# Optimization experiments

Measured on AMD Instinct MI355X. Metric: run time of the kernel, lower is better.

The kernel has to match this reference:

```python
import jax, jax.numpy as jnp
import numpy as np

B, C, H, W = 16, 3, 128, 128
PATCH = 8
E = 512          # embedding_dim
NH = 8           # num_heads
P = 64           # proj_dim
HID = 2048       # hidden_dim
L = 6            # num_layers
COND = 3
PH, PW = H // PATCH, W // PATCH
S = PH * PW + 1  # sequence length (patches + cond token)
INV_SQRT_E = 1.0 / np.float32(np.sqrt(E))

_PARAM_SHAPES = {
    'patch_w': (E, C, PATCH, PATCH), 'patch_b': (E,),
    'cond_w1': (COND, E), 'cond_b1': (E,), 'cond_w2': (E, E), 'cond_b2': (E,),
    'pos_embed': (1, S, E),
    'enc_vp': (L, NH, E, P), 'enc_kp': (L, NH, E, P), 'enc_qh': (L, NH, S, S), 'enc_lift': (L, 1, NH * P, E),
    'enc_ln1g': (L, E), 'enc_ln1b': (L, E),
    'enc_w1': (L, E, HID), 'enc_b1': (L, HID), 'enc_w2': (L, HID, E), 'enc_b2': (L, E),
    'enc_ln2g': (L, E), 'enc_ln2b': (L, E),
    'dec_vp': (L, NH, E, P), 'dec_kp': (L, NH, E, P), 'dec_qh': (L, NH, S, S), 'dec_lift': (L, 1, NH * P, E),
    'dec_ln2g': (L, E), 'dec_ln2b': (L, E),
    'dec_w1': (L, E, HID), 'dec_b1': (L, HID), 'dec_w2': (L, HID, E), 'dec_b2': (L, E),
    'dec_ln3g': (L, E), 'dec_ln3b': (L, E),
    'final_g': (E,), 'final_b': (E,),
    'deconv_w': (E, C, PATCH, PATCH), 'deconv_b': (C,),
}


def setup_inputs() -> dict:
    key = jax.random.key(0)
    inp = {
        'x': jax.random.normal(jax.random.fold_in(key, 1000), (B, C, H, W), jnp.float32),
        'y': jax.random.normal(jax.random.fold_in(key, 1001), (B, COND), jnp.float32),
    }
    for i, (name, shp) in enumerate(_PARAM_SHAPES.items()):
        w = 0.02 * jax.random.normal(jax.random.fold_in(key, i), shp, jnp.float32)
        if name.endswith('g'):  # layernorm gains near 1
            w = w + 1.0
        inp[name] = w
    return inp


def _ln(x, g, b, eps=1e-5):
    m = x.mean(-1, keepdims=True)
    v = ((x - m) ** 2).mean(-1, keepdims=True)
    return (x - m) * jax.lax.rsqrt(v + eps) * g + b


def _mhsa(x, vp, kp, qh, lift):
    # x: (B,S,E); vp/kp: (NH,E,P); qh: (NH,S,S); lift: (1, NH*P, E)
    k = jnp.einsum('bse,hep->bhsp', x, kp)
    v = jnp.einsum('bse,hep->bhsp', x, vp)
    qv = jnp.einsum('hst,bhtp->bhsp', qh, v)
    # a_ts = (qh@V) @ K^T, then transpose(-2,-1): a[t,s] = qv[s] . k[t]
    a = jnp.einsum('bhsp,bhtp->bhts', qv, k) * INV_SQRT_E
    a = jax.nn.softmax(a, axis=-1)
    o = jnp.einsum('bhst,bhtp->bhsp', a, v)          # (B,NH,S,P)
    o = o.transpose(0, 2, 1, 3).reshape(x.shape[0], S, NH * P)
    return o @ lift[0]


def _block(z, vp, kp, qh, lift, g1, b1, w1, fb1, w2, fb2, g2, b2):
    z = _ln(z + _mhsa(z, vp, kp, qh, lift), g1, b1)
    h = jax.nn.leaky_relu(z @ w1 + fb1, 0.2) @ w2 + fb2  # dropout = identity (eval)
    return _ln(z + h, g2, b2)


def reference(x, y, patch_w, patch_b, cond_w1, cond_b1, cond_w2, cond_b2, pos_embed,
              enc_vp, enc_kp, enc_qh, enc_lift, enc_ln1g, enc_ln1b,
              enc_w1, enc_b1, enc_w2, enc_b2, enc_ln2g, enc_ln2b,
              dec_vp, dec_kp, dec_qh, dec_lift, dec_ln2g, dec_ln2b,
              dec_w1, dec_b1, dec_w2, dec_b2, dec_ln3g, dec_ln3b,
              final_g, final_b, deconv_w, deconv_b):
    b = x.shape[0]
    # Patching: Conv2d(k=p, s=p) == block-reshape + einsum
    xp = x.reshape(b, C, PH, PATCH, PW, PATCH)
    tok = jnp.einsum('bchpwq,ecpq->bhwe', xp, patch_w).reshape(b, PH * PW, E) + patch_b
    cond = jax.nn.leaky_relu(y @ cond_w1 + cond_b1, 0.2)
    cond = jax.nn.leaky_relu(cond @ cond_w2 + cond_b2, 0.2)
    z = jnp.concatenate([cond[:, None, :], tok], axis=1) + pos_embed
    for i in range(L):
        z = _block(z, enc_vp[i], enc_kp[i], enc_qh[i], enc_lift[i],
                   enc_ln1g[i], enc_ln1b[i], enc_w1[i], enc_b1[i],
                   enc_w2[i], enc_b2[i], enc_ln2g[i], enc_ln2b[i])
    for i in range(L):  # decoder: only mhsa_2 / ln2 / ff / ln3 are used
        z = _block(z, dec_vp[i], dec_kp[i], dec_qh[i], dec_lift[i],
                   dec_ln2g[i], dec_ln2b[i], dec_w1[i], dec_b1[i],
                   dec_w2[i], dec_b2[i], dec_ln3g[i], dec_ln3b[i])
    z = _ln(z[:, 1:], final_g, final_b)               # drop cond token
    g = z.reshape(b, PH, PW, E)                        # (B,E,PH,PW) grid, channels-last form
    out = jnp.einsum('bhwe,ecpq->bchpwq', g, deconv_w).reshape(b, C, H, W)
    return out + deconv_b[None, :, None, None]
```

## Files before the change

### kernel.cpp

```cpp
#include <hip/hip_runtime.h>
#include <stdint.h>
#include <math.h>

#define B_    16
#define C_    3
#define HIMG  128
#define E_    512
#define NH_   8
#define S_    257
#define T_    256
#define MTOK  4096
#define MSEQ  4112
#define HID_  2048
#define SP_   288
#define SLAB  (288*288)
#define PS    2105344L
#define INV_SQRT_E 0.044194173824159216f

typedef __attribute__((ext_vector_type(8))) __bf16 bf16x8;
typedef __attribute__((ext_vector_type(4))) float f32x4;

__device__ __forceinline__ void gload16(const void* g, const void* lds)
{
    __builtin_amdgcn_global_load_lds(
        (const __attribute__((address_space(1))) uint32_t*)(uintptr_t)g,
        (__attribute__((address_space(3))) uint32_t*)(uint32_t)(uintptr_t)lds,
        16, 0, 0);
}

template<int WMW, int WNW, bool LEAKY, bool OUTF32>
__device__ __forceinline__ void gemm_core(
    const __bf16* __restrict__ A, int lda,
    const __bf16* __restrict__ Bt, int ldb,
    void* __restrict__ C, int ldc,
    const float* __restrict__ bias, float scale,
    int M, int N, int K, int tm, int tn)
{
    constexpr int BM  = WMW * 64;
    constexpr int BN  = WNW * 32;
    constexpr int T   = WMW * WNW * 64;
    constexpr int ACH = BM * 4;
    constexpr int BCH = BN * 4;
    constexpr int LPT = ACH / T + BCH / T;
    __shared__ __align__(16) __bf16 sA[4][BM * 32];
    __shared__ __align__(16) __bf16 sB[4][BN * 32];

    const int tid  = threadIdx.x;
    const int lane = tid & 63;
    const int wid  = tid >> 6;
    const int wm   = wid / WNW;
    const int wn   = wid % WNW;
    const int lh   = lane >> 4;
    const int ll   = lane & 15;

    const __bf16* Ab = A + (long)tm * BM * lda;
    const __bf16* Bb = Bt + (long)tn * BN * ldb;

    f32x4 acc[4][2] = {};
    const int nst = K >> 5;

    auto stage = [&](int buf, int k0) {
#pragma unroll
        for (int rr = 0; rr < ACH / T; ++rr) {
            const int L = rr * T + tid;
            const int row = L >> 2;
            const int gch = (L & 3) ^ ((row >> 1) & 3);
            gload16(Ab + (long)row * lda + k0 + gch * 8,
                    (const char*)(&sA[buf][0]) + (rr * T + (wid << 6)) * 16);
        }
#pragma unroll
        for (int rr = 0; rr < BCH / T; ++rr) {
            const int L = rr * T + tid;
            const int row = L >> 2;
            const int gch = (L & 3) ^ ((row >> 1) & 3);
            gload16(Bb + (long)row * ldb + k0 + gch * 8,
                    (const char*)(&sB[buf][0]) + (rr * T + (wid << 6)) * 16);
        }
    };

    const int PF = nst < 3 ? nst : 3;
    for (int s = 0; s < PF; ++s) stage(s & 3, s << 5);

    for (int st = 0; st < nst; ++st) {
        const int rem = nst - 1 - st;
        if (rem >= 2)      asm volatile("s_waitcnt vmcnt(%0)" :: "n"(2 * LPT) : "memory");
        else if (rem == 1) asm volatile("s_waitcnt vmcnt(%0)" :: "n"(LPT) : "memory");
        else               asm volatile("s_waitcnt vmcnt(0)" ::: "memory");
        __builtin_amdgcn_s_barrier();
        __builtin_amdgcn_sched_barrier(0);

        if (st + 3 < nst) stage((st + 3) & 3, (st + 3) << 5);

        const int cur = st & 3;
        bf16x8 afr[4], bfr[2];
#pragma unroll
        for (int i = 0; i < 4; ++i) {
            const int rw = wm * 64 + i * 16 + ll;
            const int c  = lh ^ ((rw >> 1) & 3);
            afr[i] = *reinterpret_cast<const bf16x8*>(&sA[cur][rw * 32 + c * 8]);
        }
#pragma unroll
        for (int j = 0; j < 2; ++j) {
            const int rw = wn * 32 + j * 16 + ll;
            const int c  = lh ^ ((rw >> 1) & 3);
            bfr[j] = *reinterpret_cast<const bf16x8*>(&sB[cur][rw * 32 + c * 8]);
        }
#pragma unroll
        for (int i = 0; i < 4; ++i)
#pragma unroll
            for (int j = 0; j < 2; ++j)
                acc[i][j] = __builtin_amdgcn_mfma_f32_16x16x32_bf16(
                                afr[i], bfr[j], acc[i][j], 0, 0, 0);
    }

#pragma unroll
    for (int i = 0; i < 4; ++i)
#pragma unroll
        for (int ii = 0; ii < 4; ++ii) {
            const int m = tm * BM + wm * 64 + i * 16 + lh * 4 + ii;
            if (m >= M) continue;
#pragma unroll
            for (int j = 0; j < 2; ++j) {
                const int n = tn * BN + wn * 32 + j * 16 + ll;
                if (n >= N) continue;
                float v = acc[i][j][ii] * scale;
                if (bias) v += bias[n];
                if (LEAKY) v = v > 0.f ? v : 0.2f * v;
                if (OUTF32) ((float*)C)[(long)m * ldc + n] = v;
                else        ((__bf16*)C)[(long)m * ldc + n] = (__bf16)v;
            }
        }
}

__device__ __forceinline__ int xcd_swizzle(int wg, int nwg)
{
    const int q = nwg >> 3, r = nwg & 7;
    if (q == 0) return wg;
    const int xcd = wg & 7, off = wg >> 3;
    return (xcd < r ? xcd * (q + 1) : r * (q + 1) + (xcd - r) * q) + off;
}

template<int WMW, int WNW, bool LEAKY, bool OUTF32>
__global__ __launch_bounds__(WMW * WNW * 64) void gemm_k(
    const __bf16* __restrict__ A, int lda, const __bf16* __restrict__ Bt, int ldb,
    void* __restrict__ C, int ldc, const float* __restrict__ bias, float scale,
    int M, int N, int K, int ntn)
{
    const int wg = xcd_swizzle(blockIdx.x, gridDim.x);
    gemm_core<WMW, WNW, LEAKY, OUTF32>(A, lda, Bt, ldb, C, ldc, bias, scale,
                                       M, N, K, wg / ntn, wg % ntn);
}

template<int WMW, int WNW>
__global__ __launch_bounds__(WMW * WNW * 64) void gemm_split_k(
    const __bf16* __restrict__ A, int lda, const __bf16* __restrict__ Bt, int ldb,
    __bf16* __restrict__ P, long pstride, const float* __restrict__ bias,
    int M, int N, int K, int npart, int ntn)
{
    const int part = blockIdx.y;
    const int Kp = K / npart;
    const int wg = xcd_swizzle(blockIdx.x, gridDim.x);
    gemm_core<WMW, WNW, false, false>(A + (long)part * Kp, lda,
                                      Bt + (long)part * Kp, ldb,
                                      P + (long)part * pstride, N,
                                      part == 0 ? bias : nullptr, 1.f,
                                      M, N, Kp, wg / ntn, wg % ntn);
}

__global__ __launch_bounds__(256) void qv_k(const __bf16* __restrict__ qhb,
                                            const __bf16* __restrict__ vT,
                                            __bf16* __restrict__ qvcat)
{
    const int bh = blockIdx.z, b = bh >> 3, h = bh & 7;
    gemm_core<2, 2, false, false>(qhb + (long)h * SLAB, SP_,
                                  vT + (long)bh * 64 * SP_, SP_,
                                  qvcat + (long)b * S_ * E_ + h * 64, E_,
                                  nullptr, 1.f, S_, 64, SP_, blockIdx.x, 0);
}

__global__ __launch_bounds__(256) void fa_k(const __bf16* __restrict__ kvcat,
                                            const __bf16* __restrict__ qvcat,
                                            const __bf16* __restrict__ vT,
                                            __bf16* __restrict__ ocat)
{
    __shared__ __align__(16) __bf16 sK[64 * 64], sQV[64 * 64], sV[64 * 64];
    __shared__ __align__(16) __bf16 sP[4][16 * 64];
    const int bh = blockIdx.y, b = bh >> 3, h = bh & 7;
    const int i0 = blockIdx.x * 64;
    const int tid = threadIdx.x, lane = tid & 63, wid = tid >> 6;
    const int ll = lane & 15, lh = lane >> 4;

    const __bf16* kSrc = kvcat + ((long)(b * S_ + i0)) * 1024 + h * 64;
    const __bf16* qvB  = qvcat + (long)b * S_ * E_ + h * 64;
    const __bf16* vTb  = vT + (long)bh * 64 * SP_;

    auto stage64 = [&](__bf16* lds, const __bf16* src, int ldsrc) {
#pragma unroll
        for (int r = 0; r < 2; ++r) {
            const int L = r * 256 + wid * 64 + lane;
            const int row = L >> 3, c = L & 7;
            const int sc = c ^ (row & 7);
            gload16(src + (long)row * ldsrc + sc * 8,
                    (const char*)lds + (r * 256 + wid * 64) * 16);
        }
    };

    stage64(sK, kSrc, 1024);
    stage64(sQV, qvB, E_);
    stage64(sV, vTb, SP_);
    __syncthreads();

    bf16x8 ka[2];
#pragma unroll
    for (int ks = 0; ks < 2; ++ks) {
        const int row = wid * 16 + ll;
        ka[ks] = *reinterpret_cast<const bf16x8*>(
            &sK[row * 64 + (((ks * 4 + lh) ^ (row & 7)) << 3)]);
    }

    float m[4], l[4];
#pragma unroll
    for (int ii = 0; ii < 4; ++ii) { m[ii] = -1e30f; l[ii] = 0.f; }
    f32x4 oacc[4] = {};

    for (int jt = 0; jt < 5; ++jt) {
        const int j0 = jt * 64;
        f32x4 s[4] = {};
#pragma unroll
        for (int ks = 0; ks < 2; ++ks)
#pragma unroll
            for (int nf = 0; nf < 4; ++nf) {
                const int row = nf * 16 + ll;
                const bf16x8 qb = *reinterpret_cast<const bf16x8*>(
                    &sQV[row * 64 + (((ks * 4 + lh) ^ (row & 7)) << 3)]);
                s[nf] = __builtin_amdgcn_mfma_f32_16x16x32_bf16(ka[ks], qb, s[nf], 0, 0, 0);
            }
        float pv[4][4];
#pragma unroll
        for (int ii = 0; ii < 4; ++ii) {
            float mx = -1e30f;
#pragma unroll
            for (int nf = 0; nf < 4; ++nf) {
                float sv = s[nf][ii] * INV_SQRT_E;
                if (j0 + nf * 16 + ll >= S_) sv = -1e30f;
                pv[nf][ii] = sv;
                mx = fmaxf(mx, sv);
            }
#pragma unroll
            for (int msk = 1; msk < 16; msk <<= 1) mx = fmaxf(mx, __shfl_xor(mx, msk));
            const float mnew = fmaxf(m[ii], mx);
            const float resc = __expf(m[ii] - mnew);
            m[ii] = mnew;
            float sum = 0.f;
#pragma unroll
            for (int nf = 0; nf < 4; ++nf) {
                const float e = __expf(pv[nf][ii] - mnew);
                pv[nf][ii] = e; sum += e;
            }
#pragma unroll
            for (int msk = 1; msk < 16; msk <<= 1) sum += __shfl_xor(sum, msk);
            l[ii] = l[ii] * resc + sum;
#pragma unroll
            for (int pf = 0; pf < 4; ++pf) oacc[pf][ii] *= resc;
        }
        __bf16* sPw = &sP[wid][0];
#pragma unroll
        for (int nf = 0; nf < 4; ++nf)
#pragma unroll
            for (int ii = 0; ii < 4; ++ii) {
                const int row = lh * 4 + ii, col = ll + 16 * nf;
                sPw[row * 64 + ((((col >> 3) ^ (row & 7)) << 3) | (col & 7))] =
                    (__bf16)pv[nf][ii];
            }
#pragma unroll
        for (int ks = 0; ks < 2; ++ks) {
            const bf16x8 pa = *reinterpret_cast<const bf16x8*>(
                &sPw[ll * 64 + (((ks * 4 + lh) ^ (ll & 7)) << 3)]);
#pragma unroll
            for (int pf = 0; pf < 4; ++pf) {
                const int row = pf * 16 + ll;
                const bf16x8 vb = *reinterpret_cast<const bf16x8*>(
                    &sV[row * 64 + (((ks * 4 + lh) ^ (row & 7)) << 3)]);
                oacc[pf] = __builtin_amdgcn_mfma_f32_16x16x32_bf16(pa, vb, oacc[pf], 0, 0, 0);
            }
        }
        if (jt < 4) {
            __syncthreads();
            stage64(sQV, qvB + (long)(j0 + 64) * E_, E_);
            stage64(sV, vTb + j0 + 64, SP_);
            __syncthreads();
        }
    }
#pragma unroll
    for (int ii = 0; ii < 4; ++ii) {
        const int i = i0 + wid * 16 + lh * 4 + ii;
        if (i >= S_) continue;
        const float invl = 1.f / l[ii];
#pragma unroll
        for (int pf = 0; pf < 4; ++pf)
            ocat[((long)(b * S_ + i)) * E_ + h * 64 + pf * 16 + ll] =
                (__bf16)(oacc[pf][ii] * invl);
    }
}

__global__ void ln_kernel(const float* __restrict__ x,
                          const __bf16* __restrict__ parts, int nparts, long pstride,
                          const float* __restrict__ g, const float* __restrict__ bb,
                          float* __restrict__ outf, __bf16* __restrict__ outb,
                          int skip_cond, int nrows)
{
    const int row = blockIdx.x * 4 + (threadIdx.x >> 6);
    if (row >= nrows) return;
    const int lane = threadIdx.x & 63;
    const long xrow = skip_cond ? (long)row + (row >> 8) + 1 : (long)row;
    const float4* xr = (const float4*)(x + xrow * E_) + lane * 2;
    const float4 a = xr[0], b4 = xr[1];
    float e[8] = {a.x, a.y, a.z, a.w, b4.x, b4.y, b4.z, b4.w};
    for (int p = 0; p < nparts; ++p) {
        const bf16x8 pv = *reinterpret_cast<const bf16x8*>(
            parts + (long)p * pstride + (long)row * E_ + lane * 8);
#pragma unroll
        for (int i = 0; i < 8; ++i) e[i] += (float)pv[i];
    }
    float s = 0.f;
#pragma unroll
    for (int i = 0; i < 8; ++i) s += e[i];
#pragma unroll
    for (int o = 32; o; o >>= 1) s += __shfl_xor(s, o);
    const float mean = s * (1.f / 512.f);
    float v = 0.f;
#pragma unroll
    for (int i = 0; i < 8; ++i) { e[i] -= mean; v += e[i] * e[i]; }
#pragma unroll
    for (int o = 32; o; o >>= 1) v += __shfl_xor(v, o);
    const float inv = rsqrtf(v * (1.f / 512.f) + 1e-5f);
    const float4* gp = (const float4*)g + lane * 2;
    const float4* bp = (const float4*)bb + lane * 2;
    const float4 g0 = gp[0], g1 = gp[1], bb0 = bp[0], bb1 = bp[1];
    const float gv[8] = {g0.x, g0.y, g0.z, g0.w, g1.x, g1.y, g1.z, g1.w};
    const float bv[8] = {bb0.x, bb0.y, bb0.z, bb0.w, bb1.x, bb1.y, bb1.z, bb1.w};
    float o8[8];
#pragma unroll
    for (int i = 0; i < 8; ++i) o8[i] = e[i] * inv * gv[i] + bv[i];
    if (outf) {
        float4* of = (float4*)(outf + (long)row * E_) + lane * 2;
        of[0] = make_float4(o8[0], o8[1], o8[2], o8[3]);
        of[1] = make_float4(o8[4], o8[5], o8[6], o8[7]);
    }
    if (outb) {
        bf16x8 ov;
#pragma unroll
        for (int i = 0; i < 8; ++i) ov[i] = (__bf16)o8[i];
        *reinterpret_cast<bf16x8*>(outb + (long)row * E_ + lane * 8) = ov;
    }
}

__global__ void conv_straight(const float* __restrict__ in, __bf16* __restrict__ out, long n)
{
    const long i = (long)blockIdx.x * 256 + threadIdx.x;
    if (i < n) out[i] = (__bf16)in[i];
}

__global__ void conv_transpose(const float* __restrict__ in, __bf16* __restrict__ out,
                               int R, int C, long in_bs, long out_bs)
{
    __shared__ float tile[32][33];
    const int bt = blockIdx.z;
    const float* ip = in + (long)bt * in_bs;
    __bf16* op = out + (long)bt * out_bs;
    const int r0 = blockIdx.x * 32, c0 = blockIdx.y * 32;
    const int tx = threadIdx.x & 31, ty = threadIdx.x >> 5;
#pragma unroll
    for (int i = 0; i < 32; i += 8) {
        const int rr = r0 + ty + i, cc = c0 + tx;
        tile[ty + i][tx] = (rr < R && cc < C) ? ip[(long)rr * C + cc] : 0.f;
    }
    __syncthreads();
#pragma unroll
    for (int i = 0; i < 32; i += 8) {
        const int cc = c0 + ty + i, rr = r0 + tx;
        if (cc < C && rr < R) op[(long)cc * R + rr] = (__bf16)tile[tx][ty + i];
    }
}

__global__ void wconv_kernel(const float* __restrict__ kp, const float* __restrict__ vp,
                             const float* __restrict__ lift, const float* __restrict__ w1,
                             const float* __restrict__ w2,
                             __bf16* __restrict__ kvT, __bf16* __restrict__ liftT,
                             __bf16* __restrict__ w1T, __bf16* __restrict__ w2T)
{
    const int j = blockIdx.y;
    const float* src; __bf16* dst; int R, C, nb;
    switch (j) {
        case 0:  src = kp;   dst = kvT;          R = 512;  C = 64;   nb = 8; break;
        case 1:  src = vp;   dst = kvT + 262144; R = 512;  C = 64;   nb = 8; break;
        case 2:  src = lift; dst = liftT;        R = 512;  C = 512;  nb = 1; break;
        case 3:  src = w1;   dst = w1T;          R = 512;  C = 2048; nb = 1; break;
        default: src = w2;   dst = w2T;          R = 2048; C = 512;  nb = 1; break;
    }
    const int tR = R >> 5, tC = C >> 5;
    int t = blockIdx.x;
    if (t >= tR * tC * nb) return;
    const int bt = t / (tR * tC);
    t %= tR * tC;
    const int rt = t / tC, ct = t % tC;
    const long bs = (long)R * C;
    const float* ip = src + (long)bt * bs;
    __bf16* op = dst + (long)bt * bs;
    __shared__ float tile[32][33];
    const int tx = threadIdx.x & 31, ty = threadIdx.x >> 5;
#pragma unroll
    for (int i = 0; i < 32; i += 8)
        tile[ty + i][tx] = ip[(long)(rt * 32 + ty + i) * C + ct * 32 + tx];
    __syncthreads();
#pragma unroll
    for (int i = 0; i < 32; i += 8)
        op[(long)(ct * 32 + ty + i) * R + rt * 32 + tx] = (__bf16)tile[tx][ty + i];
}

__global__ void conv_qh_all(const float* __restrict__ enc_qh,
                            const float* __restrict__ dec_qh,
                            __bf16* __restrict__ out)
{
    const long n = 12L * 8 * SLAB;
    for (long o = (long)blockIdx.x * 256 + threadIdx.x; o < n; o += (long)gridDim.x * 256) {
        const int t = (int)(o % SP_);
        const long rr = o / SP_;
        const int s = (int)(rr % SP_);
        const long hh = rr / SP_;
        const int h = (int)(hh % 8);
        const int lyr = (int)(hh / 8);
        float v = 0.f;
        if (s < S_ && t < S_) {
            const float* src = (lyr < 6 ? enc_qh + (long)lyr * 8 * S_ * S_
                                        : dec_qh + (long)(lyr - 6) * 8 * S_ * S_);
            v = src[((long)h * S_ + s) * S_ + t];
        }
        out[o] = (__bf16)v;
    }
}

__global__ void vtrans_kernel(const __bf16* __restrict__ kvcat, __bf16* __restrict__ vT)
{
    __shared__ __bf16 tile[32][33];
    const int bh = blockIdx.z, b = bh >> 3, h = bh & 7;
    const int t0 = blockIdx.x * 32, p0 = blockIdx.y * 32;
    const int tx = threadIdx.x & 31, ty = threadIdx.x >> 5;
#pragma unroll
    for (int i = 0; i < 32; i += 8) {
        const int t = t0 + ty + i;
        tile[ty + i][tx] = (t < S_) ?
            kvcat[((long)(b * S_ + t)) * 1024 + 512 + h * 64 + p0 + tx] : (__bf16)0.f;
    }
    __syncthreads();
#pragma unroll
    for (int i = 0; i < 32; i += 8)
        vT[(long)bh * 64 * SP_ + (long)(p0 + ty + i) * SP_ + t0 + tx] = tile[tx][ty + i];
}

__global__ void im2col_kernel(const float* __restrict__ x, __bf16* __restrict__ xcol)
{
    const int idx = blockIdx.x * 256 + threadIdx.x;
    if (idx >= MTOK * 192) return;
    const int m = idx / 192, k = idx % 192;
    const int b = m >> 8, t = m & 255;
    const int ph = t >> 4, pw = t & 15;
    const int c = k >> 6, rr = k & 63;
    const int p = rr >> 3, q = rr & 7;
    xcol[idx] = (__bf16)x[(((long)(b * C_ + c) * HIMG) + ph * 8 + p) * HIMG + pw * 8 + q];
}

__global__ void cond_kernel(const float* __restrict__ y,
                            const float* __restrict__ w1, const float* __restrict__ b1,
                            const float* __restrict__ w2, const float* __restrict__ b2,
                            const float* __restrict__ pos,
                            float* __restrict__ z, __bf16* __restrict__ zb)
{
    __shared__ float c1[512];
    const int b = blockIdx.x;
    const int e = threadIdx.x;
    float v = y[b * 3 + 0] * w1[e] + y[b * 3 + 1] * w1[512 + e]
            + y[b * 3 + 2] * w1[1024 + e] + b1[e];
    v = v > 0.f ? v : 0.2f * v;
    c1[e] = v;
    __syncthreads();
    float acc = b2[e];
    for (int k = 0; k < 512; ++k) acc += c1[k] * w2[k * 512 + e];
    acc = acc > 0.f ? acc : 0.2f * acc;
    const float o = acc + pos[e];
    z[(long)b * S_ * E_ + e] = o;
    zb[(long)b * S_ * E_ + e] = (__bf16)o;
}

__global__ void assemble_kernel(const float* __restrict__ tok,
                                const float* __restrict__ pos,
                                float* __restrict__ z, __bf16* __restrict__ zb)
{
    const int idx = blockIdx.x * 256 + threadIdx.x;
    if (idx >= MTOK * E_) return;
    const int m = idx >> 9;
    const int e = idx & 511;
    const int b = m >> 8, t = m & 255;
    const float o = tok[idx] + pos[(1 + t) * E_ + e];
    const long zi = ((long)b * S_ + 1 + t) * E_ + e;
    z[zi] = o;
    zb[zi] = (__bf16)o;
}

__global__ void scatter_kernel(const float* __restrict__ dtmp,
                               const float* __restrict__ db,
                               float* __restrict__ out)
{
    const int idx = blockIdx.x * 256 + threadIdx.x;
    if (idx >= B_ * C_ * HIMG * HIMG) return;
    const int b  = idx / (C_ * HIMG * HIMG);
    const int rm = idx % (C_ * HIMG * HIMG);
    const int c  = rm / (HIMG * HIMG);
    const int hh = (rm % (HIMG * HIMG)) / HIMG;
    const int ww = rm % HIMG;
    const int ph = hh >> 3, p = hh & 7;
    const int pw = ww >> 3, q = ww & 7;
    out[idx] = dtmp[((long)(b * 256 + ph * 16 + pw)) * 192 + c * 64 + p * 8 + q] + db[c];
}

extern "C" void kernel_launch(void* const* d_in, const int* in_sizes, int n_in,
                              void* d_out, int out_size, void* d_ws, size_t ws_size,
                              hipStream_t stream)
{
    const float* x        = (const float*)d_in[0];
    const float* y        = (const float*)d_in[1];
    const float* patch_w  = (const float*)d_in[2];
    const float* patch_b  = (const float*)d_in[3];
    const float* cond_w1  = (const float*)d_in[4];
    const float* cond_b1  = (const float*)d_in[5];
    const float* cond_w2  = (const float*)d_in[6];
    const float* cond_b2  = (const float*)d_in[7];
    const float* pos      = (const float*)d_in[8];
    const float* enc_vp   = (const float*)d_in[9];
    const float* enc_kp   = (const float*)d_in[10];
    const float* enc_qh   = (const float*)d_in[11];
    const float* enc_lift = (const float*)d_in[12];
    const float* enc_ln1g = (const float*)d_in[13];
    const float* enc_ln1b = (const float*)d_in[14];
    const float* enc_w1   = (const float*)d_in[15];
    const float* enc_b1   = (const float*)d_in[16];
    const float* enc_w2   = (const float*)d_in[17];
    const float* enc_b2   = (const float*)d_in[18];
    const float* enc_ln2g = (const float*)d_in[19];
    const float* enc_ln2b = (const float*)d_in[20];
    const float* dec_vp   = (const float*)d_in[21];
    const float* dec_kp   = (const float*)d_in[22];
    const float* dec_qh   = (const float*)d_in[23];
    const float* dec_lift = (const float*)d_in[24];
    const float* dec_ln2g = (const float*)d_in[25];
    const float* dec_ln2b = (const float*)d_in[26];
    const float* dec_w1   = (const float*)d_in[27];
    const float* dec_b1   = (const float*)d_in[28];
    const float* dec_w2   = (const float*)d_in[29];
    const float* dec_b2   = (const float*)d_in[30];
    const float* dec_ln3g = (const float*)d_in[31];
    const float* dec_ln3b = (const float*)d_in[32];
    const float* final_g  = (const float*)d_in[33];
    const float* final_b  = (const float*)d_in[34];
    const float* deconv_w = (const float*)d_in[35];
    const float* deconv_b = (const float*)d_in[36];
    float* out = (float*)d_out;

    char* wp = (char*)d_ws;
    auto alloc_f32 = [&](long n) { float* p = (float*)wp; wp += ((n * 4 + 63) & ~63LL); return p; };
    auto alloc_bf  = [&](long n) { __bf16* p = (__bf16*)wp; wp += ((n * 2 + 63) & ~63LL); return p; };

    float*  z      = alloc_f32(2105344);
    float*  tok    = alloc_f32(2097152);
    float*  dtmp   = alloc_f32(786432);
    __bf16* zb     = alloc_bf(4352L * 512);
    __bf16* xcolb  = alloc_bf(786432);
    __bf16* kvcat  = alloc_bf(4352L * 1024);
    __bf16* qvcat  = alloc_bf(4352L * 512);
    __bf16* ocat   = alloc_bf(4352L * 512);
    __bf16* vT     = alloc_bf(128L * 64 * SP_);
    __bf16* psl    = alloc_bf(4L * PS);
    __bf16* hidden = alloc_bf(4224L * 2048);
    __bf16* gbuf   = alloc_bf(4096L * 512);
    __bf16* pwb    = alloc_bf(512L * 192);
    __bf16* dwTb   = alloc_bf(192L * 512);
    __bf16* kvTb   = alloc_bf(1024L * 512);
    __bf16* liftTb = alloc_bf(262144);
    __bf16* w1Tb   = alloc_bf(1048576);
    __bf16* w2Tb   = alloc_bf(1048576);
    __bf16* qhb12  = alloc_bf(12L * 8 * SLAB + 96L * SP_);
    (void)ws_size; (void)in_sizes; (void)n_in; (void)out_size;

    const dim3 blk(256);

    conv_straight<<<dim3(384), blk, 0, stream>>>(patch_w, pwb, 98304);
    conv_transpose<<<dim3(16, 6, 1), blk, 0, stream>>>(deconv_w, dwTb, 512, 192, 0, 0);
    conv_qh_all<<<dim3(4096), blk, 0, stream>>>(enc_qh, dec_qh, qhb12);

    im2col_kernel<<<dim3(3072), blk, 0, stream>>>(x, xcolb);
    gemm_k<2, 2, false, true><<<dim3(256), blk, 0, stream>>>(
        xcolb, 192, pwb, 192, tok, 512, patch_b, 1.f, MTOK, 512, 192, 8);
    cond_kernel<<<dim3(B_), dim3(512), 0, stream>>>(y, cond_w1, cond_b1,
                                                    cond_w2, cond_b2, pos, z, zb);
    assemble_kernel<<<dim3(8192), blk, 0, stream>>>(tok, pos, z, zb);

    for (int l = 0; l < 12; ++l) {
        const bool enc = l < 6;
        const int  li  = enc ? l : l - 6;
        const float* vp   = (enc ? enc_vp   : dec_vp)   + (long)li * NH_ * E_ * 64;
        const float* kp   = (enc ? enc_kp   : dec_kp)   + (long)li * NH_ * E_ * 64;
        const float* lift = (enc ? enc_lift : dec_lift) + (long)li * 512 * 512;
        const float* g1   = (enc ? enc_ln1g : dec_ln2g) + li * E_;
        const float* bb1  = (enc ? enc_ln1b : dec_ln2b) + li * E_;
        const float* w1   = (enc ? enc_w1   : dec_w1)   + (long)li * E_ * HID_;
        const float* fb1  = (enc ? enc_b1   : dec_b1)   + li * HID_;
        const float* w2   = (enc ? enc_w2   : dec_w2)   + (long)li * HID_ * E_;
        const float* fb2  = (enc ? enc_b2   : dec_b2)   + li * E_;
        const float* g2   = (enc ? enc_ln2g : dec_ln3g) + li * E_;
        const float* bb2  = (enc ? enc_ln2b : dec_ln3b) + li * E_;
        const __bf16* qhb = qhb12 + (long)l * 8 * SLAB;

        wconv_kernel<<<dim3(1024, 5), blk, 0, stream>>>(kp, vp, lift, w1, w2,
                                                        kvTb, liftTb, w1Tb, w2Tb);

        gemm_k<2, 2, false, false><<<dim3(528), blk, 0, stream>>>(
            zb, 512, kvTb, 512, kvcat, 1024, nullptr, 1.f, MSEQ, 1024, 512, 16);
        vtrans_kernel<<<dim3(9, 2, 128), blk, 0, stream>>>(kvcat, vT);
        qv_k<<<dim3(3, 1, 128), blk, 0, stream>>>(qhb, vT, qvcat);
        fa_k<<<dim3(5, 128), blk, 0, stream>>>(kvcat, qvcat, vT, ocat);
        gemm_split_k<2, 2><<<dim3(264, 2), blk, 0, stream>>>(
            ocat, 512, liftTb, 512, psl, PS, nullptr, MSEQ, 512, 512, 2, 8);
        ln_kernel<<<dim3(1028), blk, 0, stream>>>(z, psl, 2, PS, g1, bb1,
                                                  z, zb, 0, MSEQ);

        gemm_k<2, 2, true, false><<<dim3(1056), blk, 0, stream>>>(
            zb, 512, w1Tb, 512, hidden, 2048, fb1, 1.f, MSEQ, HID_, 512, 32);
        gemm_split_k<2, 2><<<dim3(264, 4), blk, 0, stream>>>(
            hidden, 2048, w2Tb, 2048, psl, PS, fb2, MSEQ, 512, HID_, 4, 8);
        ln_kernel<<<dim3(1028), blk, 0, stream>>>(z, psl, 4, PS, g2, bb2,
                                                  z, zb, 0, MSEQ);
    }

    ln_kernel<<<dim3(1024), blk, 0, stream>>>(z, nullptr, 0, 0, final_g, final_b,
                                              nullptr, gbuf, 1, MTOK);
    gemm_k<2, 2, false, true><<<dim3(96), blk, 0, stream>>>(
        gbuf, 512, dwTb, 512, dtmp, 192, nullptr, 1.f, MTOK, 192, 512, 3);
    scatter_kernel<<<dim3(3072), blk, 0, stream>>>(dtmp, deconv_b, out);
}
```

Baseline: 1.576 ms.

## Fuse V transpose into KV GEMM, batch weight conversion, drop fp32 residual

The KV projection GEMM now writes V directly in transposed, padded layout, which removes the separate vtrans kernel and halves the K/V scratch buffer. A one-time vpad kernel zeroes the pad columns. Weight conversion for all 12 layers moves into a single up-front launch instead of one launch per layer. The fp32 residual stream z is removed, and LayerNorm reads and writes the residual in bf16 only, which cuts memory traffic but loses residual precision across 12 layers. The fused V stores are scattered with a row stride of 288, so they are poorly coalesced.

```diff
diff --git a/kernel.cpp b/kernel.cpp
--- a/kernel.cpp
+++ b/kernel.cpp
@@ -28,13 +28,13 @@
         16, 0, 0);
 }
 
-template<int WMW, int WNW, bool LEAKY, bool OUTF32>
+template<int WMW, int WNW, bool LEAKY, bool OUTF32, bool VSPLIT>
 __device__ __forceinline__ void gemm_core(
     const __bf16* __restrict__ A, int lda,
     const __bf16* __restrict__ Bt, int ldb,
     void* __restrict__ C, int ldc,
     const float* __restrict__ bias, float scale,
-    int M, int N, int K, int tm, int tn)
+    int M, int N, int K, int tm, int tn, __bf16* __restrict__ vTout)
 {
     constexpr int BM  = WMW * 64;
     constexpr int BN  = WNW * 32;
@@ -126,8 +126,17 @@
                 float v = acc[i][j][ii] * scale;
                 if (bias) v += bias[n];
                 if (LEAKY) v = v > 0.f ? v : 0.2f * v;
-                if (OUTF32) ((float*)C)[(long)m * ldc + n] = v;
-                else        ((__bf16*)C)[(long)m * ldc + n] = (__bf16)v;
+                if (VSPLIT && n >= 512) {
+                    const int b = m / S_;
+                    const int t = m - b * S_;
+                    const int hp = n - 512;
+                    vTout[(((long)(b * 8 + (hp >> 6)) * 64) + (hp & 63)) * SP_ + t] =
+                        (__bf16)v;
+                } else if (OUTF32) {
+                    ((float*)C)[(long)m * ldc + n] = v;
+                } else {
+                    ((__bf16*)C)[(long)m * ldc + n] = (__bf16)v;
+                }
             }
         }
 }
@@ -140,15 +149,15 @@
     return (xcd < r ? xcd * (q + 1) : r * (q + 1) + (xcd - r) * q) + off;
 }
 
-template<int WMW, int WNW, bool LEAKY, bool OUTF32>
+template<int WMW, int WNW, bool LEAKY, bool OUTF32, bool VSPLIT>
 __global__ __launch_bounds__(WMW * WNW * 64) void gemm_k(
     const __bf16* __restrict__ A, int lda, const __bf16* __restrict__ Bt, int ldb,
     void* __restrict__ C, int ldc, const float* __restrict__ bias, float scale,
-    int M, int N, int K, int ntn)
+    int M, int N, int K, int ntn, __bf16* __restrict__ vTout)
 {
     const int wg = xcd_swizzle(blockIdx.x, gridDim.x);
-    gemm_core<WMW, WNW, LEAKY, OUTF32>(A, lda, Bt, ldb, C, ldc, bias, scale,
-                                       M, N, K, wg / ntn, wg % ntn);
+    gemm_core<WMW, WNW, LEAKY, OUTF32, VSPLIT>(A, lda, Bt, ldb, C, ldc, bias, scale,
+                                               M, N, K, wg / ntn, wg % ntn, vTout);
 }
 
 template<int WMW, int WNW>
@@ -160,11 +169,11 @@
     const int part = blockIdx.y;
     const int Kp = K / npart;
     const int wg = xcd_swizzle(blockIdx.x, gridDim.x);
-    gemm_core<WMW, WNW, false, false>(A + (long)part * Kp, lda,
-                                      Bt + (long)part * Kp, ldb,
-                                      P + (long)part * pstride, N,
-                                      part == 0 ? bias : nullptr, 1.f,
-                                      M, N, Kp, wg / ntn, wg % ntn);
+    gemm_core<WMW, WNW, false, false, false>(A + (long)part * Kp, lda,
+                                             Bt + (long)part * Kp, ldb,
+                                             P + (long)part * pstride, N,
+                                             part == 0 ? bias : nullptr, 1.f,
+                                             M, N, Kp, wg / ntn, wg % ntn, nullptr);
 }
 
 __global__ __launch_bounds__(256) void qv_k(const __bf16* __restrict__ qhb,
@@ -172,13 +181,14 @@
                                             __bf16* __restrict__ qvcat)
 {
     const int bh = blockIdx.z, b = bh >> 3, h = bh & 7;
-    gemm_core<2, 2, false, false>(qhb + (long)h * SLAB, SP_,
-                                  vT + (long)bh * 64 * SP_, SP_,
-                                  qvcat + (long)b * S_ * E_ + h * 64, E_,
-                                  nullptr, 1.f, S_, 64, SP_, blockIdx.x, 0);
-}
-
-__global__ __launch_bounds__(256) void fa_k(const __bf16* __restrict__ kvcat,
+    gemm_core<2, 2, false, false, false>(qhb + (long)h * SLAB, SP_,
+                                         vT + (long)bh * 64 * SP_, SP_,
+                                         qvcat + (long)b * S_ * E_ + h * 64, E_,
+                                         nullptr, 1.f, S_, 64, SP_, blockIdx.x, 0,
+                                         nullptr);
+}
+
+__global__ __launch_bounds__(256) void fa_k(const __bf16* __restrict__ kcat,
                                             const __bf16* __restrict__ qvcat,
                                             const __bf16* __restrict__ vT,
                                             __bf16* __restrict__ ocat)
@@ -190,7 +200,7 @@
     const int tid = threadIdx.x, lane = tid & 63, wid = tid >> 6;
     const int ll = lane & 15, lh = lane >> 4;
 
-    const __bf16* kSrc = kvcat + ((long)(b * S_ + i0)) * 1024 + h * 64;
+    const __bf16* kSrc = kcat + ((long)(b * S_ + i0)) * 512 + h * 64;
     const __bf16* qvB  = qvcat + (long)b * S_ * E_ + h * 64;
     const __bf16* vTb  = vT + (long)bh * 64 * SP_;
 
@@ -205,7 +215,7 @@
         }
     };
 
-    stage64(sK, kSrc, 1024);
+    stage64(sK, kSrc, 512);
     stage64(sQV, qvB, E_);
     stage64(sV, vTb, SP_);
     __syncthreads();
@@ -303,19 +313,19 @@
     }
 }
 
-__global__ void ln_kernel(const float* __restrict__ x,
+__global__ void ln_kernel(const __bf16* x,
                           const __bf16* __restrict__ parts, int nparts, long pstride,
                           const float* __restrict__ g, const float* __restrict__ bb,
-                          float* __restrict__ outf, __bf16* __restrict__ outb,
-                          int skip_cond, int nrows)
+                          __bf16* outb, int skip_cond, int nrows)
 {
     const int row = blockIdx.x * 4 + (threadIdx.x >> 6);
     if (row >= nrows) return;
     const int lane = threadIdx.x & 63;
     const long xrow = skip_cond ? (long)row + (row >> 8) + 1 : (long)row;
-    const float4* xr = (const float4*)(x + xrow * E_) + lane * 2;
-    const float4 a = xr[0], b4 = xr[1];
-    float e[8] = {a.x, a.y, a.z, a.w, b4.x, b4.y, b4.z, b4.w};
+    const bf16x8 xa = *reinterpret_cast<const bf16x8*>(x + xrow * E_ + lane * 8);
+    float e[8];
+#pragma unroll
+    for (int i = 0; i < 8; ++i) e[i] = (float)xa[i];
     for (int p = 0; p < nparts; ++p) {
         const bf16x8 pv = *reinterpret_cast<const bf16x8*>(
             parts + (long)p * pstride + (long)row * E_ + lane * 8);
@@ -339,20 +349,10 @@
     const float4 g0 = gp[0], g1 = gp[1], bb0 = bp[0], bb1 = bp[1];
     const float gv[8] = {g0.x, g0.y, g0.z, g0.w, g1.x, g1.y, g1.z, g1.w};
     const float bv[8] = {bb0.x, bb0.y, bb0.z, bb0.w, bb1.x, bb1.y, bb1.z, bb1.w};
-    float o8[8];
-#pragma unroll
-    for (int i = 0; i < 8; ++i) o8[i] = e[i] * inv * gv[i] + bv[i];
-    if (outf) {
-        float4* of = (float4*)(outf + (long)row * E_) + lane * 2;
-        of[0] = make_float4(o8[0], o8[1], o8[2], o8[3]);
-        of[1] = make_float4(o8[4], o8[5], o8[6], o8[7]);
-    }
-    if (outb) {
-        bf16x8 ov;
-#pragma unroll
-        for (int i = 0; i < 8; ++i) ov[i] = (__bf16)o8[i];
-        *reinterpret_cast<bf16x8*>(outb + (long)row * E_ + lane * 8) = ov;
-    }
+    bf16x8 ov;
+#pragma unroll
+    for (int i = 0; i < 8; ++i) ov[i] = (__bf16)(e[i] * inv * gv[i] + bv[i]);
+    *reinterpret_cast<bf16x8*>(outb + (long)row * E_ + lane * 8) = ov;
 }
 
 __global__ void conv_straight(const float* __restrict__ in, __bf16* __restrict__ out, long n)
@@ -362,41 +362,48 @@
 }
 
 __global__ void conv_transpose(const float* __restrict__ in, __bf16* __restrict__ out,
-                               int R, int C, long in_bs, long out_bs)
+                               int R, int C)
 {
     __shared__ float tile[32][33];
-    const int bt = blockIdx.z;
-    const float* ip = in + (long)bt * in_bs;
-    __bf16* op = out + (long)bt * out_bs;
     const int r0 = blockIdx.x * 32, c0 = blockIdx.y * 32;
     const int tx = threadIdx.x & 31, ty = threadIdx.x >> 5;
 #pragma unroll
     for (int i = 0; i < 32; i += 8) {
         const int rr = r0 + ty + i, cc = c0 + tx;
-        tile[ty + i][tx] = (rr < R && cc < C) ? ip[(long)rr * C + cc] : 0.f;
+        tile[ty + i][tx] = (rr < R && cc < C) ? in[(long)rr * C + cc] : 0.f;
     }
     __syncthreads();
 #pragma unroll
     for (int i = 0; i < 32; i += 8) {
         const int cc = c0 + ty + i, rr = r0 + tx;
-        if (cc < C && rr < R) op[(long)cc * R + rr] = (__bf16)tile[tx][ty + i];
-    }
-}
-
-__global__ void wconv_kernel(const float* __restrict__ kp, const float* __restrict__ vp,
-                             const float* __restrict__ lift, const float* __restrict__ w1,
-                             const float* __restrict__ w2,
-                             __bf16* __restrict__ kvT, __bf16* __restrict__ liftT,
-                             __bf16* __restrict__ w1T, __bf16* __restrict__ w2T)
-{
+        if (cc < C && rr < R) out[(long)cc * R + rr] = (__bf16)tile[tx][ty + i];
+    }
+}
+
+__global__ void wconv_all(const float* __restrict__ enc_kp, const float* __restrict__ dec_kp,
+                          const float* __restrict__ enc_vp, const float* __restrict__ dec_vp,
+                          const float* __restrict__ enc_lift, const float* __restrict__ dec_lift,
+                          const float* __restrict__ enc_w1, const float* __restrict__ dec_w1,
+                          const float* __restrict__ enc_w2, const float* __restrict__ dec_w2,
+                          __bf16* __restrict__ kvT, __bf16* __restrict__ liftT,
+                          __bf16* __restrict__ w1T, __bf16* __restrict__ w2T)
+{
+    const int lyr = blockIdx.z;
+    const bool enc = lyr < 6;
+    const int li = enc ? lyr : lyr - 6;
     const int j = blockIdx.y;
     const float* src; __bf16* dst; int R, C, nb;
     switch (j) {
-        case 0:  src = kp;   dst = kvT;          R = 512;  C = 64;   nb = 8; break;
-        case 1:  src = vp;   dst = kvT + 262144; R = 512;  C = 64;   nb = 8; break;
-        case 2:  src = lift; dst = liftT;        R = 512;  C = 512;  nb = 1; break;
-        case 3:  src = w1;   dst = w1T;          R = 512;  C = 2048; nb = 1; break;
-        default: src = w2;   dst = w2T;          R = 2048; C = 512;  nb = 1; break;
+        case 0:  src = (enc ? enc_kp : dec_kp) + (long)li * 262144;
+                 dst = kvT + (long)lyr * 524288;            R = 512; C = 64;   nb = 8; break;
+        case 1:  src = (enc ? enc_vp : dec_vp) + (long)li * 262144;
+                 dst = kvT + (long)lyr * 524288 + 262144;   R = 512; C = 64;   nb = 8; break;
+        case 2:  src = (enc ? enc_lift : dec_lift) + (long)li * 262144;
+                 dst = liftT + (long)lyr * 262144;          R = 512; C = 512;  nb = 1; break;
+        case 3:  src = (enc ? enc_w1 : dec_w1) + (long)li * 1048576;
+                 dst = w1T + (long)lyr * 1048576;           R = 512; C = 2048; nb = 1; break;
+        default: src = (enc ? enc_w2 : dec_w2) + (long)li * 1048576;
+                 dst = w2T + (long)lyr * 1048576;           R = 2048; C = 512; nb = 1; break;
     }
     const int tR = R >> 5, tC = C >> 5;
     int t = blockIdx.x;
@@ -440,22 +447,13 @@
     }
 }
 
-__global__ void vtrans_kernel(const __bf16* __restrict__ kvcat, __bf16* __restrict__ vT)
-{
-    __shared__ __bf16 tile[32][33];
-    const int bh = blockIdx.z, b = bh >> 3, h = bh & 7;
-    const int t0 = blockIdx.x * 32, p0 = blockIdx.y * 32;
-    const int tx = threadIdx.x & 31, ty = threadIdx.x >> 5;
-#pragma unroll
-    for (int i = 0; i < 32; i += 8) {
-        const int t = t0 + ty + i;
-        tile[ty + i][tx] = (t < S_) ?
-            kvcat[((long)(b * S_ + t)) * 1024 + 512 + h * 64 + p0 + tx] : (__bf16)0.f;
-    }
-    __syncthreads();
-#pragma unroll
-    for (int i = 0; i < 32; i += 8)
-        vT[(long)bh * 64 * SP_ + (long)(p0 + ty + i) * SP_ + t0 + tx] = tile[tx][ty + i];
+__global__ void vpad_kernel(__bf16* __restrict__ vT)
+{
+    const int i = blockIdx.x * 256 + threadIdx.x;
+    if (i >= 128 * 64 * 31) return;
+    const int t = 257 + (i % 31);
+    const long rp = i / 31;
+    vT[rp * SP_ + t] = (__bf16)0.f;
 }
 
 __global__ void im2col_kernel(const float* __restrict__ x, __bf16* __restrict__ xcol)
@@ -473,8 +471,7 @@
 __global__ void cond_kernel(const float* __restrict__ y,
                             const float* __restrict__ w1, const float* __restrict__ b1,
                             const float* __restrict__ w2, const float* __restrict__ b2,
-                            const float* __restrict__ pos,
-                            float* __restrict__ z, __bf16* __restrict__ zb)
+                            const float* __restrict__ pos, __bf16* __restrict__ zb)
 {
     __shared__ float c1[512];
     const int b = blockIdx.x;
@@ -487,24 +484,20 @@
     float acc = b2[e];
     for (int k = 0; k < 512; ++k) acc += c1[k] * w2[k * 512 + e];
     acc = acc > 0.f ? acc : 0.2f * acc;
-    const float o = acc + pos[e];
-    z[(long)b * S_ * E_ + e] = o;
-    zb[(long)b * S_ * E_ + e] = (__bf16)o;
-}
-
-__global__ void assemble_kernel(const float* __restrict__ tok,
+    zb[(long)b * S_ * E_ + e] = (__bf16)(acc + pos[e]);
+}
+
+__global__ void assemble_kernel(const __bf16* __restrict__ tok,
                                 const float* __restrict__ pos,
-                                float* __restrict__ z, __bf16* __restrict__ zb)
+                                __bf16* __restrict__ zb)
 {
     const int idx = blockIdx.x * 256 + threadIdx.x;
     if (idx >= MTOK * E_) return;
     const int m = idx >> 9;
     const int e = idx & 511;
     const int b = m >> 8, t = m & 255;
-    const float o = tok[idx] + pos[(1 + t) * E_ + e];
-    const long zi = ((long)b * S_ + 1 + t) * E_ + e;
-    z[zi] = o;
-    zb[zi] = (__bf16)o;
+    const float o = (float)tok[idx] + pos[(1 + t) * E_ + e];
+    zb[((long)b * S_ + 1 + t) * E_ + e] = (__bf16)o;
 }
 
 __global__ void scatter_kernel(const float* __restrict__ dtmp,
@@ -570,12 +563,11 @@
     auto alloc_f32 = [&](long n) { float* p = (float*)wp; wp += ((n * 4 + 63) & ~63LL); return p; };
     auto alloc_bf  = [&](long n) { __bf16* p = (__bf16*)wp; wp += ((n * 2 + 63) & ~63LL); return p; };
 
-    float*  z      = alloc_f32(2105344);
-    float*  tok    = alloc_f32(2097152);
     float*  dtmp   = alloc_f32(786432);
     __bf16* zb     = alloc_bf(4352L * 512);
+    __bf16* tok    = alloc_bf(4096L * 512);
     __bf16* xcolb  = alloc_bf(786432);
-    __bf16* kvcat  = alloc_bf(4352L * 1024);
+    __bf16* kcat   = alloc_bf(4352L * 512);
     __bf16* qvcat  = alloc_bf(4352L * 512);
     __bf16* ocat   = alloc_bf(4352L * 512);
     __bf16* vT     = alloc_bf(128L * 64 * SP_);
@@ -584,66 +576,65 @@
     __bf16* gbuf   = alloc_bf(4096L * 512);
     __bf16* pwb    = alloc_bf(512L * 192);
     __bf16* dwTb   = alloc_bf(192L * 512);
-    __bf16* kvTb   = alloc_bf(1024L * 512);
-    __bf16* liftTb = alloc_bf(262144);
-    __bf16* w1Tb   = alloc_bf(1048576);
-    __bf16* w2Tb   = alloc_bf(1048576);
+    __bf16* kvT12  = alloc_bf(12L * 524288);
+    __bf16* liftT12= alloc_bf(12L * 262144);
+    __bf16* w1T12  = alloc_bf(12L * 1048576);
+    __bf16* w2T12  = alloc_bf(12L * 1048576);
     __bf16* qhb12  = alloc_bf(12L * 8 * SLAB + 96L * SP_);
     (void)ws_size; (void)in_sizes; (void)n_in; (void)out_size;
 
     const dim3 blk(256);
 
     conv_straight<<<dim3(384), blk, 0, stream>>>(patch_w, pwb, 98304);
-    conv_transpose<<<dim3(16, 6, 1), blk, 0, stream>>>(deconv_w, dwTb, 512, 192, 0, 0);
+    conv_transpose<<<dim3(16, 6), blk, 0, stream>>>(deconv_w, dwTb, 512, 192);
+    wconv_all<<<dim3(1024, 5, 12), blk, 0, stream>>>(
+        enc_kp, dec_kp, enc_vp, dec_vp, enc_lift, dec_lift,
+        enc_w1, dec_w1, enc_w2, dec_w2, kvT12, liftT12, w1T12, w2T12);
     conv_qh_all<<<dim3(4096), blk, 0, stream>>>(enc_qh, dec_qh, qhb12);
+    vpad_kernel<<<dim3(992), blk, 0, stream>>>(vT);
 
     im2col_kernel<<<dim3(3072), blk, 0, stream>>>(x, xcolb);
-    gemm_k<2, 2, false, true><<<dim3(256), blk, 0, stream>>>(
-        xcolb, 192, pwb, 192, tok, 512, patch_b, 1.f, MTOK, 512, 192, 8);
+    gemm_k<2, 2, false, false, false><<<dim3(256), blk, 0, stream>>>(
+        xcolb, 192, pwb, 192, tok, 512, patch_b, 1.f, MTOK, 512, 192, 8, nullptr);
     cond_kernel<<<dim3(B_), dim3(512), 0, stream>>>(y, cond_w1, cond_b1,
-                                                    cond_w2, cond_b2, pos, z, zb);
-    assemble_kernel<<<dim3(8192), blk, 0, stream>>>(tok, pos, z, zb);
+                                                    cond_w2, cond_b2, pos, zb);
+    assemble_kernel<<<dim3(8192), blk, 0, stream>>>(tok, pos, zb);
 
     for (int l = 0; l < 12; ++l) {
         const bool enc = l < 6;
         const int  li  = enc ? l : l - 6;
-        const float* vp   = (enc ? enc_vp   : dec_vp)   + (long)li * NH_ * E_ * 64;
-        const float* kp   = (enc ? enc_kp   : dec_kp)   + (long)li * NH_ * E_ * 64;
-        const float* lift = (enc ? enc_lift : dec_lift) + (long)li * 512 * 512;
         const float* g1   = (enc ? enc_ln1g : dec_ln2g) + li * E_;
         const float* bb1  = (enc ? enc_ln1b : dec_ln2b) + li * E_;
-        const float* w1   = (enc ? enc_w1   : dec_w1)   + (long)li * E_ * HID_;
         const float* fb1  = (enc ? enc_b1   : dec_b1)   + li * HID_;
-        const float* w2   = (enc ? enc_w2   : dec_w2)   + (long)li * HID_ * E_;
         const float* fb2  = (enc ? enc_b2   : dec_b2)   + li * E_;
         const float* g2   = (enc ? enc_ln2g : dec_ln3g) + li * E_;
         const float* bb2  = (enc ? enc_ln2b : dec_ln3b) + li * E_;
-        const __bf16* qhb = qhb12 + (long)l * 8 * SLAB;
-
-        wconv_kernel<<<dim3(1024, 5), blk, 0, stream>>>(kp, vp, lift, w1, w2,
-                                                        kvTb, liftTb, w1Tb, w2Tb);
-
-        gemm_k<2, 2, false, false><<<dim3(528), blk, 0, stream>>>(
-            zb, 512, kvTb, 512, kvcat, 1024, nullptr, 1.f, MSEQ, 1024, 512, 16);
-        vtrans_kernel<<<dim3(9, 2, 128), blk, 0, stream>>>(kvcat, vT);
+        const __bf16* kvTb   = kvT12 + (long)l * 524288;
+        const __bf16* liftTb = liftT12 + (long)l * 262144;
+        const __bf16* w1Tb   = w1T12 + (long)l * 1048576;
+        const __bf16* w2Tb   = w2T12 + (long)l * 1048576;
+        const __bf16* qhb    = qhb12 + (long)l * 8 * SLAB;
+
+        gemm_k<2, 2, false, false, true><<<dim3(528), blk, 0, stream>>>(
+            zb, 512, kvTb, 512, kcat, 512, nullptr, 1.f, MSEQ, 1024, 512, 16, vT);
         qv_k<<<dim3(3, 1, 128), blk, 0, stream>>>(qhb, vT, qvcat);
-        fa_k<<<dim3(5, 128), blk, 0, stream>>>(kvcat, qvcat, vT, ocat);
+        fa_k<<<dim3(5, 128), blk, 0, stream>>>(kcat, qvcat, vT, ocat);
         gemm_split_k<2, 2><<<dim3(264, 2), blk, 0, stream>>>(
             ocat, 512, liftTb, 512, psl, PS, nullptr, MSEQ, 512, 512, 2, 8);
-        ln_kernel<<<dim3(1028), blk, 0, stream>>>(z, psl, 2, PS, g1, bb1,
-                                                  z, zb, 0, MSEQ);
-
-        gemm_k<2, 2, true, false><<<dim3(1056), blk, 0, stream>>>(
-            zb, 512, w1Tb, 512, hidden, 2048, fb1, 1.f, MSEQ, HID_, 512, 32);
+        ln_kernel<<<dim3(1028), blk, 0, stream>>>(zb, psl, 2, PS, g1, bb1,
+                                                  zb, 0, MSEQ);
+
+        gemm_k<2, 2, true, false, false><<<dim3(1056), blk, 0, stream>>>(
+            zb, 512, w1Tb, 512, hidden, 2048, fb1, 1.f, MSEQ, HID_, 512, 32, nullptr);
         gemm_split_k<2, 2><<<dim3(264, 4), blk, 0, stream>>>(
             hidden, 2048, w2Tb, 2048, psl, PS, fb2, MSEQ, 512, HID_, 4, 8);
-        ln_kernel<<<dim3(1028), blk, 0, stream>>>(z, psl, 4, PS, g2, bb2,
-                                                  z, zb, 0, MSEQ);
-    }
-
-    ln_kernel<<<dim3(1024), blk, 0, stream>>>(z, nullptr, 0, 0, final_g, final_b,
-                                              nullptr, gbuf, 1, MTOK);
-    gemm_k<2, 2, false, true><<<dim3(96), blk, 0, stream>>>(
-        gbuf, 512, dwTb, 512, dtmp, 192, nullptr, 1.f, MTOK, 192, 512, 3);
+        ln_kernel<<<dim3(1028), blk, 0, stream>>>(zb, psl, 4, PS, g2, bb2,
+                                                  zb, 0, MSEQ);
+    }
+
+    ln_kernel<<<dim3(1024), blk, 0, stream>>>(zb, nullptr, 0, 0, final_g, final_b,
+                                              gbuf, 1, MTOK);
+    gemm_k<2, 2, false, true, false><<<dim3(96), blk, 0, stream>>>(
+        gbuf, 512, dwTb, 512, dtmp, 192, nullptr, 1.f, MTOK, 192, 512, 3, nullptr);
     scatter_kernel<<<dim3(3072), blk, 0, stream>>>(dtmp, deconv_b, out);
 }
```

Result: faster. 1.527 ms (-3.1%).
